# Optimization experiments

Measured on AMD Instinct MI355X. Metric: run time of the kernel, lower is better.

## Reference

```python
import jax, jax.numpy as jnp
import numpy as np

LLR_CLIP = 20.0   # allowed_llr_range(abs=20)
QMAX = 7.5        # decoder_qms_qbit = 5 -> round(x*2)/2, clip +/-7.5


def _quantize_ste(x):
    # straight-through quantizer: forward = quantized, grad flows through clipped x
    q = jnp.clip(jnp.round(x * 2.0) / 2.0, -QMAX, QMAX)
    xc = jnp.clip(x, -QMAX, QMAX)
    return xc + jax.lax.stop_gradient(q - xc)


def _decode(xa, cn_weights, vn_idx, cn_idx, shifts, M):
    # xa: (B, Z, N) channel LLRs; messages live on lifted edges (B, Z, E)
    B, Z, N = xa.shape
    E = vn_idx.shape[0]
    iters = cn_weights.shape[0]

    zidx = jnp.arange(Z)
    lift = (zidx[:, None] + shifts[None, :]) % Z    # VN-domain -> CN-domain cyclic shift per edge
    unlift = (zidx[:, None] - shifts[None, :]) % Z  # inverse shift
    lift_b = jnp.broadcast_to(lift[None], (B, Z, E))
    unlift_b = jnp.broadcast_to(unlift[None], (B, Z, E))

    V = jax.nn.one_hot(vn_idx, N, dtype=xa.dtype)   # (E, N) edge->VN incidence (= W_output / W_skipconn2even)
    eids = jnp.arange(E)
    llr_e = xa[:, :, vn_idx]                        # per-edge channel LLR (B, Z, E)

    c2v = jnp.zeros((B, Z, E), xa.dtype)
    for it in range(iters):
        # --- VN update (odd layer): extrinsic sum + channel LLR, clipped ---
        tot = jnp.einsum('bze,en->bzn', c2v, V)                 # per-VN sum of incoming c2v
        v2c = jnp.clip(llr_e + tot[:, :, vn_idx] - c2v, -LLR_CLIP, LLR_CLIP)

        # --- lift to CN domain (Lift_Matrix1) ---
        m = jnp.take_along_axis(v2c, lift_b, axis=1)            # (B, Z, E)
        mt = m.transpose(2, 0, 1).reshape(E, B * Z)             # edges leading for segment ops

        # --- CN update (even layer): extrinsic min-sum via two-min trick ---
        a = jnp.abs(mt)
        neg = (mt < 0).astype(jnp.int32)
        min1 = jax.ops.segment_min(a, cn_idx, num_segments=M)               # (M, B*Z)
        ismin = a == min1[cn_idx]
        first = jax.ops.segment_min(jnp.where(ismin, eids[:, None], E),
                                    cn_idx, num_segments=M)                 # tie-break by edge id
        isfirst = eids[:, None] == first[cn_idx]
        min2 = jax.ops.segment_min(jnp.where(isfirst, jnp.inf, a),
                                   cn_idx, num_segments=M)
        ext_min = jnp.where(isfirst, min2[cn_idx], min1[cn_idx])
        negtot = jax.ops.segment_sum(neg, cn_idx, num_segments=M)
        sgn = (1 - 2 * ((negtot[cn_idx] - neg) % 2)).astype(mt.dtype)       # extrinsic sign product

        msg = _quantize_ste(cn_weights[it] * sgn * ext_min)     # per-iteration scalar CN weight + QMS quantize

        # --- unlift back to VN domain (Lift_Matrix2) ---
        mc = msg.reshape(E, B, Z).transpose(1, 2, 0)
        c2v = jnp.take_along_axis(mc, unlift_b, axis=1)

    # marginal output LLRs (W_output): channel + all incoming c2v, shape (B, N*Z)
    out = xa + jnp.einsum('bze,en->bzn', c2v, V)
    return out.transpose(0, 2, 1).reshape(B, N * Z)


def setup_inputs() -> dict:
    key = jax.random.key(0)
    B, Z, N, M, dc = 32, 384, 68, 46, 7
    E = M * dc  # 322
    k1, k2, k3 = jax.random.split(key, 3)
    xa = jax.random.normal(k1, (B, Z, N), dtype=jnp.float32) * 4.0
    cn_weights = jnp.ones((8,), jnp.float32)
    cn_idx = jnp.repeat(jnp.arange(M), dc)                      # regular CN degree 7
    vn_idx = jax.random.randint(k2, (E,), 0, N)
    shifts = jax.random.randint(k3, (E,), 0, Z)
    return {"xa": xa, "cn_weights": cn_weights, "vn_idx": vn_idx,
            "cn_idx": cn_idx, "shifts": shifts, "M": M}


def reference(xa, cn_weights, vn_idx, cn_idx, shifts, M):
    return _decode(xa, cn_weights, vn_idx, cn_idx, shifts, M)
```

## Files before the change

kernel.cpp:

```cpp
#include <hip/hip_runtime.h>

#define B_   32
#define Z_   384
#define N_   68
#define M_   46
#define DC_  7
#define E_   (M_ * DC_)
#define ZN   (Z_ * N_)
#define ZM   (Z_ * M_)
#define MSB  (DC_ * ZM)

#define XAT_OFF   0
#define LT_OFF    (B_ * ZN)
#define MSG_OFF   (2 * B_ * ZN)
#define MSG_INTS  ((B_ * MSB + 3) / 4)
#define EVS_OFF   (MSG_OFF + MSG_INTS)
#define OFFS_OFF  (EVS_OFF + E_)
#define LST_OFF   (OFFS_OFF + N_ + 1)
#define WS_INTS   (LST_OFF + E_)


__global__ __launch_bounds__(384)
void k_pre_tables(const float* __restrict__ xa,
                  const int* __restrict__ vn_idx, const int* __restrict__ shifts,
                  int* __restrict__ ws, float* __restrict__ xat_dst)
{
    const int tid = threadIdx.x;
    if (blockIdx.x == B_ * 6) {
        __shared__ int vnl[E_];
        __shared__ int shl[E_];
        __shared__ int offs[N_ + 1];
        if (tid < E_) { vnl[tid] = vn_idx[tid]; shl[tid] = shifts[tid]; }
        __syncthreads();
        if (tid < N_) {
            int c = 0;
            for (int e = 0; e < E_; ++e) c += (vnl[e] == tid);
            offs[tid + 1] = c;
        }
        if (tid == 0) offs[0] = 0;
        __syncthreads();
        if (tid == 0) { for (int n = 0; n < N_; ++n) offs[n + 1] += offs[n]; }
        __syncthreads();
        if (tid < E_) {
            ws[EVS_OFF + tid] = (vnl[tid] * Z_ << 9) | shl[tid];
        }
        if (tid < N_ + 1) ws[OFFS_OFF + tid] = offs[tid];
        if (tid < N_) {
            int p = offs[tid];
            for (int e = 0; e < E_; ++e) {
                if (vnl[e] == tid) {
                    int m = e / DC_, j = e - m * DC_;
                    ws[LST_OFF + p++] = ((j * ZM + m * Z_) << 9) | shl[e];
                }
            }
        }
        return;
    }
    __shared__ float tile[N_ * 65];
    const int x = blockIdx.x & 7;
    const int k = blockIdx.x >> 3;
    const int b = x + 8 * (k & 3);
    const int t = k >> 2;
    const int z0 = t * 64;
    const float* src = xa + (size_t)b * ZN + (size_t)z0 * N_;
    for (int i = tid; i < 64 * N_; i += 384) {
        int r = i / N_, n = i - r * N_;
        tile[n * 65 + r] = src[i];
    }
    __syncthreads();
    float* dst = xat_dst + (size_t)b * ZN + z0;
    for (int i = tid; i < 64 * N_; i += 384) {
        int n = i >> 6, zl = i & 63;
        dst[n * Z_ + zl] = tile[n * 65 + zl];
    }
}

__global__ __launch_bounds__(384)
void k_passB(const float* __restrict__ cw, const int* __restrict__ ws_tbl,
             signed char* __restrict__ msg, const float* __restrict__ src_g,
             int it, int use_init)
{
    __shared__ int cevs[DC_];
    const int x = blockIdx.x & 7;
    const int k = blockIdx.x >> 3;
    const int b = x + 8 * (k & 3);
    const int m = k >> 2;
    const int z = threadIdx.x;
    if (z < DC_) cevs[z] = ws_tbl[EVS_OFF + m * DC_ + z];
    __syncthreads();

    const float* src = src_g + (size_t)b * ZN;
    signed char* mp = msg + (size_t)b * MSB + m * Z_ + z;
    const float w = cw[it];

    float m1 = 1e30f, m2 = 1e30f;
    int f = 0, negb = 0;
    #pragma unroll
    for (int j = 0; j < DC_; ++j) {
        int rec = cevs[j];
        int s = rec & 511;
        int zr = z + s; if (zr >= Z_) zr -= Z_;
        int c2 = use_init ? 0 : (int)mp[j * ZM];
        float v = src[(rec >> 9) + zr] - 0.5f * (float)c2;
        v = fminf(fmaxf(v, -20.0f), 20.0f);
        negb |= (v < 0.0f) << j;
        float a = fabsf(v);
        if (a < m1) { m2 = m1; m1 = a; f = j; }
        else if (a < m2) { m2 = a; }
    }
    float r1 = fminf(fmaxf(rintf(w * m1 * 2.0f), -15.0f), 15.0f);
    float r2 = fminf(fmaxf(rintf(w * m2 * 2.0f), -15.0f), 15.0f);
    const int q1 = (int)r1, q2 = (int)r2;
    const int par = __popc(negb);
    #pragma unroll
    for (int j = 0; j < DC_; ++j) {
        int q  = (j == f) ? q2 : q1;
        int sj = (par - ((negb >> j) & 1)) & 1;
        mp[j * ZM] = (signed char)(sj ? -q : q);
    }
}

__global__ __launch_bounds__(384)
void k_passA(const float* __restrict__ xat, const int* __restrict__ ws_tbl,
             const signed char* __restrict__ msg, float* __restrict__ dst)
{
    __shared__ int vlist[16];
    __shared__ int s_cnt;
    const int x = blockIdx.x & 7;
    const int k = blockIdx.x >> 3;
    const int b = x + 8 * (k & 3);
    const int n = k >> 2;
    const int tid = threadIdx.x;
    const int o = ws_tbl[OFFS_OFF + n];
    const int e = ws_tbl[OFFS_OFF + n + 1];
    if (tid == 0) s_cnt = e - o;
    if (tid < e - o && tid < 16) vlist[tid] = ws_tbl[LST_OFF + o + tid];
    __syncthreads();

    const int z = tid;
    const signed char* mb = msg + (size_t)b * MSB;
    const int cnt = s_cnt;
    int t2 = 0;
    for (int q = 0; q < cnt; ++q) {
        int rec = (q < 16) ? vlist[q] : ws_tbl[LST_OFF + o + q];
        int s = rec & 511;
        int zs = z - s; if (zs < 0) zs += Z_;
        t2 += (int)mb[(rec >> 9) + zs];
    }
    dst[(size_t)b * ZN + n * Z_ + z] =
        xat[(size_t)b * ZN + n * Z_ + z] + 0.5f * (float)t2;
}

#define INIT_STATE ((16u << 10) | (16u << 15))
__device__ __forceinline__ int decode2(unsigned st, int j) {
    int neg   = (st >> j) & 1;
    int q1    = (int)((st >> 10) & 31) - 16;
    int q2    = (int)((st >> 15) & 31) - 16;
    int first = (int)((st >> 7) & 7);
    int q     = (j == first) ? q2 : q1;
    int par   = (__popc(st & 127u) - neg) & 1;
    return par ? -q : q;
}

__global__ __launch_bounds__(1024)
void ldpc_decode_kernel(const float* __restrict__ xa,
                        const float* __restrict__ cw,
                        const int*   __restrict__ vn_idx,
                        const int*   __restrict__ shifts,
                        float* out, int iters)
{
    __shared__ short tot[ZN];
    __shared__ int   evs[E_];
    __shared__ int   offs[N_ + 1];
    __shared__ int   lists[E_];
    __shared__ float wlds[8];

    const int tid = threadIdx.x;
    const int b   = blockIdx.x;
    const float* xab = xa + (size_t)b * ZN;
    float* outb = out + (size_t)b * ZN;
    int* stateg = (int*)outb;

    if (tid < E_) evs[tid] = vn_idx[tid] | (shifts[tid] << 7);
    if (tid < iters && tid < 8) wlds[tid] = cw[tid];
    __syncthreads();
    if (tid < N_) {
        int c = 0;
        for (int e = 0; e < E_; ++e) c += ((evs[e] & 127) == tid);
        offs[tid + 1] = c;
    }
    if (tid == 0) offs[0] = 0;
    __syncthreads();
    if (tid == 0) { for (int n = 0; n < N_; ++n) offs[n + 1] += offs[n]; }
    __syncthreads();
    if (tid < N_) {
        int p = offs[tid];
        for (int e = 0; e < E_; ++e) {
            int rec = evs[e];
            if ((rec & 127) == tid) {
                int s = rec >> 7;
                lists[p++] = s | ((e / DC_) << 9) | ((e % DC_) << 15);
            }
        }
    }
    __syncthreads();

    for (int i = tid; i < ZM; i += 1024) stateg[i] = (int)INIT_STATE;
    __syncthreads();

    for (int it = 0; it < iters; ++it) {
        for (int i = tid; i < ZN; i += 1024) {
            int z = i / N_, n = i - z * N_, t2 = 0;
            int kend = offs[n + 1];
            for (int k = offs[n]; k < kend; ++k) {
                int rec = lists[k];
                int s = rec & 511, m = (rec >> 9) & 63, j = rec >> 15;
                int zs = z - s; if (zs < 0) zs += Z_;
                t2 += decode2((unsigned)stateg[zs * M_ + m], j);
            }
            tot[i] = (short)t2;
        }
        __syncthreads();
        const float w = wlds[it];
        for (int i = tid; i < ZM; i += 1024) {
            int z = i / M_, m = i - z * M_;
            unsigned st = (unsigned)stateg[i];
            float m1 = 1e30f, m2 = 1e30f;
            int f = 0, negb = 0;
            #pragma unroll
            for (int j = 0; j < DC_; ++j) {
                int rec = evs[m * DC_ + j];
                int vn = rec & 127, s = rec >> 7;
                int zr = z + s; if (zr >= Z_) zr -= Z_;
                int c2 = decode2(st, j);
                int idx = zr * N_ + vn;
                float v = (xab[idx] + 0.5f * (float)tot[idx]) - 0.5f * (float)c2;
                v = fminf(fmaxf(v, -20.0f), 20.0f);
                negb |= (v < 0.0f) << j;
                float a = fabsf(v);
                if (a < m1) { m2 = m1; m1 = a; f = j; }
                else if (a < m2) { m2 = a; }
            }
            float r1 = fminf(fmaxf(rintf(w * m1 * 2.0f), -15.0f), 15.0f);
            float r2 = fminf(fmaxf(rintf(w * m2 * 2.0f), -15.0f), 15.0f);
            stateg[i] = (int)(unsigned)(negb | (f << 7) | (((int)r1 + 16) << 10) | (((int)r2 + 16) << 15));
        }
        __syncthreads();
    }

    for (int i = tid; i < ZN; i += 1024) {
        int z = i / N_, n = i - z * N_, t2 = 0;
        int kend = offs[n + 1];
        for (int k = offs[n]; k < kend; ++k) {
            int rec = lists[k];
            int s = rec & 511, m = (rec >> 9) & 63, j = rec >> 15;
            int zs = z - s; if (zs < 0) zs += Z_;
            t2 += decode2((unsigned)stateg[zs * M_ + m], j);
        }
        tot[i] = (short)t2;
    }
    __syncthreads();
    for (int i = tid; i < ZN; i += 1024) {
        int n = i / Z_, z = i - n * Z_;
        outb[i] = xab[z * N_ + n] + 0.5f * (float)tot[z * N_ + n];
    }
}

extern "C" void kernel_launch(void* const* d_in, const int* in_sizes, int n_in,
                              void* d_out, int out_size, void* d_ws, size_t ws_size,
                              hipStream_t stream) {
    const float* xa = (const float*)d_in[0];
    const float* cw = (const float*)d_in[1];
    const int* vn   = (const int*)d_in[2];
    const int* sh   = (const int*)d_in[4];
    int iters = in_sizes[1];
    float* outp = (float*)d_out;

    if (ws_size >= (size_t)WS_INTS * sizeof(int)) {
        int*         ws  = (int*)d_ws;
        float*       xat = (float*)d_ws + XAT_OFF;
        float*       lt  = (float*)d_ws + LT_OFF;
        signed char* msg = (signed char*)(ws + MSG_OFF);

        if (iters == 0) {
            hipLaunchKernelGGL(k_pre_tables, dim3(B_ * 6 + 1), dim3(384), 0, stream,
                               xa, vn, sh, ws, outp);
            return;
        }
        hipLaunchKernelGGL(k_pre_tables, dim3(B_ * 6 + 1), dim3(384), 0, stream,
                           xa, vn, sh, ws, xat);
        hipLaunchKernelGGL(k_passB, dim3(B_ * M_), dim3(384), 0, stream,
                           cw, ws, msg, xat, 0, 1);
        for (int it = 1; it < iters; ++it) {
            hipLaunchKernelGGL(k_passA, dim3(B_ * N_), dim3(384), 0, stream,
                               xat, ws, msg, lt);
            hipLaunchKernelGGL(k_passB, dim3(B_ * M_), dim3(384), 0, stream,
                               cw, ws, msg, lt, it, 0);
        }
        hipLaunchKernelGGL(k_passA, dim3(B_ * N_), dim3(384), 0, stream,
                           xat, ws, msg, outp);
    } else {
        hipLaunchKernelGGL(ldpc_decode_kernel, dim3(B_), dim3(1024), 0, stream,
                           xa, cw, vn, sh, outp, iters);
    }
}
```

Measured before the change: 201.5 us.

## Fuse VN and CN updates into one per-iteration kernel with double-buffered messages

Replaces the separate per-iteration VN-sum pass and CN pass with a single kernel. For each edge it recomputes the variable-node total on the fly from int8 messages, using a precomputed per-check table of neighbour edges and relative shifts. Messages are double-buffered across iterations. Table building, the transpose and iteration 0 are folded into one initial kernel. This halves kernel launches and removes the float intermediate round trip through memory, at the cost of redundant gathers of the VN sums per edge.

```diff
diff --git a/kernel.cpp b/kernel.cpp
--- a/kernel.cpp
+++ b/kernel.cpp
@@ -10,53 +10,219 @@
 #define ZM   (Z_ * M_)
 #define MSB  (DC_ * ZM)
 
-#define XAT_OFF   0
-#define LT_OFF    (B_ * ZN)
-#define MSG_OFF   (2 * B_ * ZN)
-#define MSG_INTS  ((B_ * MSB + 3) / 4)
-#define EVS_OFF   (MSG_OFF + MSG_INTS)
-#define OFFS_OFF  (EVS_OFF + E_)
-#define LST_OFF   (OFFS_OFF + N_ + 1)
-#define WS_INTS   (LST_OFF + E_)
+#define MAXDV   20
+#define JSTRIDE (2 + MAXDV)
+#define CSTRIDE (DC_ * JSTRIDE)
+#define W_XAT   0
+#define MSG_INTS ((B_ * MSB + 3) / 4)
+#define W_MSG0  (B_ * ZN)
+#define W_MSG1  (W_MSG0 + MSG_INTS)
+#define W_OFFS  (W_MSG1 + MSG_INTS)
+#define W_LST   (W_OFFS + N_ + 1)
+#define W_CHK   (W_LST + E_)
+#define W_INTS  (W_CHK + M_ * CSTRIDE)
 
 
 __global__ __launch_bounds__(384)
-void k_pre_tables(const float* __restrict__ xa,
-                  const int* __restrict__ vn_idx, const int* __restrict__ shifts,
-                  int* __restrict__ ws, float* __restrict__ xat_dst)
-{
-    const int tid = threadIdx.x;
-    if (blockIdx.x == B_ * 6) {
-        __shared__ int vnl[E_];
-        __shared__ int shl[E_];
-        __shared__ int offs[N_ + 1];
+void k_it0(const float* __restrict__ xa, const float* __restrict__ cw,
+           const int* __restrict__ vn_idx, const int* __restrict__ shifts,
+           int* __restrict__ ws, signed char* __restrict__ msg )
+{
+    __shared__ float tile[N_ * 65];
+    __shared__ int cvn[DC_];
+    __shared__ int csh[DC_];
+    __shared__ int vnl[E_];
+    __shared__ int shl[E_];
+    __shared__ int offsS[N_ + 1];
+    __shared__ int lstS[E_];
+
+    const int tid = threadIdx.x;
+    const int x = blockIdx.x & 7;
+    const int k = blockIdx.x >> 3;
+    const int b = x + 8 * (k & 3);
+    const int m = k >> 2;
+    const int z = tid;
+
+    if (tid < DC_) { cvn[tid] = vn_idx[m * DC_ + tid]; csh[tid] = shifts[m * DC_ + tid]; }
+    __syncthreads();
+
+    const float* xab = xa + (size_t)b * ZN;
+    const float w = cw[0];
+    float m1 = 1e30f, m2 = 1e30f;
+    int f = 0, negb = 0;
+    #pragma unroll
+    for (int j = 0; j < DC_; ++j) {
+        int zr = z + csh[j]; if (zr >= Z_) zr -= Z_;
+        float v = xab[(size_t)zr * N_ + cvn[j]];
+        v = fminf(fmaxf(v, -20.0f), 20.0f);
+        negb |= (v < 0.0f) << j;
+        float a = fabsf(v);
+        if (a < m1) { m2 = m1; m1 = a; f = j; }
+        else if (a < m2) { m2 = a; }
+    }
+    float r1 = fminf(fmaxf(rintf(w * m1 * 2.0f), -15.0f), 15.0f);
+    float r2 = fminf(fmaxf(rintf(w * m2 * 2.0f), -15.0f), 15.0f);
+    const int q1 = (int)r1, q2 = (int)r2;
+    const int par = __popc(negb);
+    signed char* mp = msg + (size_t)b * MSB + m * Z_ + z;
+    #pragma unroll
+    for (int j = 0; j < DC_; ++j) {
+        int q  = (j == f) ? q2 : q1;
+        int sj = (par - ((negb >> j) & 1)) & 1;
+        mp[j * ZM] = (signed char)(sj ? -q : q);
+    }
+
+    if (m < 6) {
+        const int z0 = m * 64;
+        const float* src = xab + (size_t)z0 * N_;
+        for (int i = tid; i < 64 * N_; i += 384) {
+            int r = i / N_, n = i - r * N_;
+            tile[n * 65 + r] = src[i];
+        }
+        __syncthreads();
+        float* xat = (float*)(ws + W_XAT) + (size_t)b * ZN + z0;
+        for (int i = tid; i < 64 * N_; i += 384) {
+            int n = i >> 6, zl = i & 63;
+            xat[n * Z_ + zl] = tile[n * 65 + zl];
+        }
+    }
+
+    if (b == 0 && m == 6) {
         if (tid < E_) { vnl[tid] = vn_idx[tid]; shl[tid] = shifts[tid]; }
         __syncthreads();
         if (tid < N_) {
             int c = 0;
             for (int e = 0; e < E_; ++e) c += (vnl[e] == tid);
-            offs[tid + 1] = c;
-        }
-        if (tid == 0) offs[0] = 0;
-        __syncthreads();
-        if (tid == 0) { for (int n = 0; n < N_; ++n) offs[n + 1] += offs[n]; }
-        __syncthreads();
-        if (tid < E_) {
-            ws[EVS_OFF + tid] = (vnl[tid] * Z_ << 9) | shl[tid];
-        }
-        if (tid < N_ + 1) ws[OFFS_OFF + tid] = offs[tid];
+            offsS[tid + 1] = c;
+        }
+        if (tid == 0) offsS[0] = 0;
+        __syncthreads();
+        if (tid == 0) { for (int n = 0; n < N_; ++n) offsS[n + 1] += offsS[n]; }
+        __syncthreads();
         if (tid < N_) {
-            int p = offs[tid];
+            int p = offsS[tid];
             for (int e = 0; e < E_; ++e) {
                 if (vnl[e] == tid) {
-                    int m = e / DC_, j = e - m * DC_;
-                    ws[LST_OFF + p++] = ((j * ZM + m * Z_) << 9) | shl[e];
+                    int mm = e / DC_, j = e - mm * DC_;
+                    int rec = ((j * ZM + mm * Z_) << 9) | shl[e];
+                    lstS[p] = rec;
+                    ws[W_LST + p] = rec;
+                    ++p;
                 }
             }
         }
-        return;
-    }
+        if (tid < N_ + 1) ws[W_OFFS + tid] = offsS[tid];
+        __syncthreads();
+        if (tid < E_) {
+            int mm = tid / DC_, j = tid - mm * DC_;
+            int vn = vnl[tid], sj = shl[tid];
+            int* dst = ws + W_CHK + mm * CSTRIDE + j * JSTRIDE;
+            dst[0] = (vn * Z_ << 9) | sj;
+            int o = offsS[vn];
+            int dv = offsS[vn + 1] - o;
+            if (dv > MAXDV) dv = MAXDV;
+            dst[1] = dv;
+            for (int q = 0; q < dv; ++q) {
+                int r = lstS[o + q];
+                int sc = sj - (r & 511);
+                if (sc < 0) sc += Z_;
+                dst[2 + q] = (r & ~511) | sc;
+            }
+        }
+    }
+}
+
+__global__ __launch_bounds__(384)
+void k_fit(const float* __restrict__ cw, const int* __restrict__ ws,
+           const signed char* __restrict__ mold, signed char* __restrict__ mnew,
+           int it)
+{
+    __shared__ int stbl[CSTRIDE];
+    const int tid = threadIdx.x;
+    const int x = blockIdx.x & 7;
+    const int k = blockIdx.x >> 3;
+    const int b = x + 8 * (k & 3);
+    const int m = k >> 2;
+    const int z = tid;
+    for (int i = tid; i < CSTRIDE; i += 384) stbl[i] = ws[W_CHK + m * CSTRIDE + i];
+    __syncthreads();
+
+    const float* xb = (const float*)(ws + W_XAT) + (size_t)b * ZN;
+    const signed char* mo = mold + (size_t)b * MSB;
+    const float w = cw[it];
+
+    float m1 = 1e30f, m2 = 1e30f;
+    int f = 0, negb = 0;
+    #pragma unroll
+    for (int j = 0; j < DC_; ++j) {
+        const int rec = stbl[j * JSTRIDE];
+        int zr = z + (rec & 511); if (zr >= Z_) zr -= Z_;
+        float v = xb[(rec >> 9) + zr];
+        const int dv = stbl[j * JSTRIDE + 1];
+        int t2 = 0;
+        for (int q = 0; q < dv; ++q) {
+            int r = stbl[j * JSTRIDE + 2 + q];
+            int zs = z + (r & 511); if (zs >= Z_) zs -= Z_;
+            t2 += (int)mo[(r >> 9) + zs];
+        }
+        int c2 = (int)mo[j * ZM + m * Z_ + z];
+        float lt = v + 0.5f * (float)t2;
+        v = lt - 0.5f * (float)c2;
+        v = fminf(fmaxf(v, -20.0f), 20.0f);
+        negb |= (v < 0.0f) << j;
+        float a = fabsf(v);
+        if (a < m1) { m2 = m1; m1 = a; f = j; }
+        else if (a < m2) { m2 = a; }
+    }
+    float r1 = fminf(fmaxf(rintf(w * m1 * 2.0f), -15.0f), 15.0f);
+    float r2 = fminf(fmaxf(rintf(w * m2 * 2.0f), -15.0f), 15.0f);
+    const int q1 = (int)r1, q2 = (int)r2;
+    const int par = __popc(negb);
+    signed char* mn = mnew + (size_t)b * MSB + m * Z_ + z;
+    #pragma unroll
+    for (int j = 0; j < DC_; ++j) {
+        int q  = (j == f) ? q2 : q1;
+        int sj = (par - ((negb >> j) & 1)) & 1;
+        mn[j * ZM] = (signed char)(sj ? -q : q);
+    }
+}
+
+__global__ __launch_bounds__(384)
+void k_out(const int* __restrict__ ws, const signed char* __restrict__ msg,
+           float* __restrict__ dst)
+{
+    __shared__ int vlist[16];
+    __shared__ int s_cnt;
+    const int x = blockIdx.x & 7;
+    const int k = blockIdx.x >> 3;
+    const int b = x + 8 * (k & 3);
+    const int n = k >> 2;
+    const int tid = threadIdx.x;
+    const int o = ws[W_OFFS + n];
+    const int e = ws[W_OFFS + n + 1];
+    if (tid == 0) s_cnt = e - o;
+    if (tid < e - o && tid < 16) vlist[tid] = ws[W_LST + o + tid];
+    __syncthreads();
+
+    const int z = tid;
+    const signed char* mb = msg + (size_t)b * MSB;
+    const float* xb = (const float*)(ws + W_XAT) + (size_t)b * ZN;
+    const int cnt = s_cnt;
+    int t2 = 0;
+    for (int q = 0; q < cnt; ++q) {
+        int rec = (q < 16) ? vlist[q] : ws[W_LST + o + q];
+        int s = rec & 511;
+        int zs = z - s; if (zs < 0) zs += Z_;
+        t2 += (int)mb[(rec >> 9) + zs];
+    }
+    dst[(size_t)b * ZN + n * Z_ + z] = xb[n * Z_ + z] + 0.5f * (float)t2;
+}
+
+__global__ __launch_bounds__(384)
+void k_tr(const float* __restrict__ xa, float* __restrict__ dst_g)
+{
     __shared__ float tile[N_ * 65];
+    const int tid = threadIdx.x;
     const int x = blockIdx.x & 7;
     const int k = blockIdx.x >> 3;
     const int b = x + 8 * (k & 3);
@@ -68,87 +234,11 @@
         tile[n * 65 + r] = src[i];
     }
     __syncthreads();
-    float* dst = xat_dst + (size_t)b * ZN + z0;
+    float* dst = dst_g + (size_t)b * ZN + z0;
     for (int i = tid; i < 64 * N_; i += 384) {
         int n = i >> 6, zl = i & 63;
         dst[n * Z_ + zl] = tile[n * 65 + zl];
     }
-}
-
-__global__ __launch_bounds__(384)
-void k_passB(const float* __restrict__ cw, const int* __restrict__ ws_tbl,
-             signed char* __restrict__ msg, const float* __restrict__ src_g,
-             int it, int use_init)
-{
-    __shared__ int cevs[DC_];
-    const int x = blockIdx.x & 7;
-    const int k = blockIdx.x >> 3;
-    const int b = x + 8 * (k & 3);
-    const int m = k >> 2;
-    const int z = threadIdx.x;
-    if (z < DC_) cevs[z] = ws_tbl[EVS_OFF + m * DC_ + z];
-    __syncthreads();
-
-    const float* src = src_g + (size_t)b * ZN;
-    signed char* mp = msg + (size_t)b * MSB + m * Z_ + z;
-    const float w = cw[it];
-
-    float m1 = 1e30f, m2 = 1e30f;
-    int f = 0, negb = 0;
-    #pragma unroll
-    for (int j = 0; j < DC_; ++j) {
-        int rec = cevs[j];
-        int s = rec & 511;
-        int zr = z + s; if (zr >= Z_) zr -= Z_;
-        int c2 = use_init ? 0 : (int)mp[j * ZM];
-        float v = src[(rec >> 9) + zr] - 0.5f * (float)c2;
-        v = fminf(fmaxf(v, -20.0f), 20.0f);
-        negb |= (v < 0.0f) << j;
-        float a = fabsf(v);
-        if (a < m1) { m2 = m1; m1 = a; f = j; }
-        else if (a < m2) { m2 = a; }
-    }
-    float r1 = fminf(fmaxf(rintf(w * m1 * 2.0f), -15.0f), 15.0f);
-    float r2 = fminf(fmaxf(rintf(w * m2 * 2.0f), -15.0f), 15.0f);
-    const int q1 = (int)r1, q2 = (int)r2;
-    const int par = __popc(negb);
-    #pragma unroll
-    for (int j = 0; j < DC_; ++j) {
-        int q  = (j == f) ? q2 : q1;
-        int sj = (par - ((negb >> j) & 1)) & 1;
-        mp[j * ZM] = (signed char)(sj ? -q : q);
-    }
-}
-
-__global__ __launch_bounds__(384)
-void k_passA(const float* __restrict__ xat, const int* __restrict__ ws_tbl,
-             const signed char* __restrict__ msg, float* __restrict__ dst)
-{
-    __shared__ int vlist[16];
-    __shared__ int s_cnt;
-    const int x = blockIdx.x & 7;
-    const int k = blockIdx.x >> 3;
-    const int b = x + 8 * (k & 3);
-    const int n = k >> 2;
-    const int tid = threadIdx.x;
-    const int o = ws_tbl[OFFS_OFF + n];
-    const int e = ws_tbl[OFFS_OFF + n + 1];
-    if (tid == 0) s_cnt = e - o;
-    if (tid < e - o && tid < 16) vlist[tid] = ws_tbl[LST_OFF + o + tid];
-    __syncthreads();
-
-    const int z = tid;
-    const signed char* mb = msg + (size_t)b * MSB;
-    const int cnt = s_cnt;
-    int t2 = 0;
-    for (int q = 0; q < cnt; ++q) {
-        int rec = (q < 16) ? vlist[q] : ws_tbl[LST_OFF + o + q];
-        int s = rec & 511;
-        int zs = z - s; if (zs < 0) zs += Z_;
-        t2 += (int)mb[(rec >> 9) + zs];
-    }
-    dst[(size_t)b * ZN + n * Z_ + z] =
-        xat[(size_t)b * ZN + n * Z_ + z] + 0.5f * (float)t2;
 }
 
 #define INIT_STATE ((16u << 10) | (16u << 15))
@@ -276,29 +366,26 @@
     int iters = in_sizes[1];
     float* outp = (float*)d_out;
 
-    if (ws_size >= (size_t)WS_INTS * sizeof(int)) {
-        int*         ws  = (int*)d_ws;
-        float*       xat = (float*)d_ws + XAT_OFF;
-        float*       lt  = (float*)d_ws + LT_OFF;
-        signed char* msg = (signed char*)(ws + MSG_OFF);
+    if (ws_size >= (size_t)W_INTS * sizeof(int)) {
+        int*         ws   = (int*)d_ws;
+        signed char* msg0 = (signed char*)(ws + W_MSG0);
+        signed char* msg1 = (signed char*)(ws + W_MSG1);
 
         if (iters == 0) {
-            hipLaunchKernelGGL(k_pre_tables, dim3(B_ * 6 + 1), dim3(384), 0, stream,
-                               xa, vn, sh, ws, outp);
+            hipLaunchKernelGGL(k_tr, dim3(B_ * 6), dim3(384), 0, stream, xa, outp);
             return;
         }
-        hipLaunchKernelGGL(k_pre_tables, dim3(B_ * 6 + 1), dim3(384), 0, stream,
-                           xa, vn, sh, ws, xat);
-        hipLaunchKernelGGL(k_passB, dim3(B_ * M_), dim3(384), 0, stream,
-                           cw, ws, msg, xat, 0, 1);
+        hipLaunchKernelGGL(k_it0, dim3(B_ * M_), dim3(384), 0, stream,
+                           xa, cw, vn, sh, ws, msg0);
         for (int it = 1; it < iters; ++it) {
-            hipLaunchKernelGGL(k_passA, dim3(B_ * N_), dim3(384), 0, stream,
-                               xat, ws, msg, lt);
-            hipLaunchKernelGGL(k_passB, dim3(B_ * M_), dim3(384), 0, stream,
-                               cw, ws, msg, lt, it, 0);
-        }
-        hipLaunchKernelGGL(k_passA, dim3(B_ * N_), dim3(384), 0, stream,
-                           xat, ws, msg, outp);
+            signed char* wbuf = (it & 1) ? msg1 : msg0;
+            signed char* rbuf = (it & 1) ? msg0 : msg1;
+            hipLaunchKernelGGL(k_fit, dim3(B_ * M_), dim3(384), 0, stream,
+                               cw, ws, rbuf, wbuf, it);
+        }
+        signed char* fin = ((iters - 1) & 1) ? msg1 : msg0;
+        hipLaunchKernelGGL(k_out, dim3(B_ * N_), dim3(384), 0, stream,
+                           ws, fin, outp);
     } else {
         hipLaunchKernelGGL(ldpc_decode_kernel, dim3(B_), dim3(1024), 0, stream,
                            xa, cw, vn, sh, outp, iters);
```

After: 221.9 us. 10.1% more time.
